# Kernel tuning notes

Hardware: AMD Instinct MI355X
Metric: run time of the kernel (lower is better)

Reference implementation:

```python
import jax, jax.numpy as jnp
import numpy as np

B, H, W = 4, 128, 128
DIM, HEADS, WS, SS = 192, 6, 16, 8
CAT, NTOK, RD, DTD = 128, 64, 10, 64
MLPH, KSZ = 384, 5
LN_EPS = 1e-5


def _ln(x, g, b):
    mu = jnp.mean(x, axis=-1, keepdims=True)
    var = jnp.mean((x - mu) ** 2, axis=-1, keepdims=True)
    return (x - mu) * jax.lax.rsqrt(var + LN_EPS) * g + b


def _l2n(x):
    n = jnp.sqrt(jnp.sum(x * x, axis=-1, keepdims=True))
    return x / jnp.maximum(n, 1e-12)


def _win_part(x, ws):
    b, h, w, c = x.shape
    x = x.reshape(b, h // ws, ws, w // ws, ws, c).transpose(0, 1, 3, 2, 4, 5)
    return x.reshape(-1, ws, ws, c)


def _win_rev(win, ws, h, w):
    b = win.shape[0] // ((h // ws) * (w // ws))
    x = win.reshape(b, h // ws, w // ws, ws, ws, -1).transpose(0, 1, 3, 2, 4, 5)
    return x.reshape(b, h, w, -1)


def _make_rpi(ws):
    coords = np.stack(np.meshgrid(np.arange(ws), np.arange(ws), indexing='ij'))
    cf = coords.reshape(2, -1)
    rel = (cf[:, :, None] - cf[:, None, :]).transpose(1, 2, 0)
    rel[:, :, 0] += ws - 1
    rel[:, :, 1] += ws - 1
    rel[:, :, 0] *= 2 * ws - 1
    return rel.sum(-1)


def _make_attn_mask(h, w, ws, ss):
    img = np.zeros((1, h, w, 1), np.float32)
    cnt = 0
    for hs in (slice(0, -ws), slice(-ws, -ss), slice(-ss, None)):
        for vs in (slice(0, -ws), slice(-ws, -ss), slice(-ss, None)):
            img[:, hs, vs, :] = cnt
            cnt += 1
    mw = img.reshape(1, h // ws, ws, w // ws, ws, 1).transpose(0, 1, 3, 2, 4, 5).reshape(-1, ws * ws)
    am = mw[:, None, :] - mw[:, :, None]
    return np.where(am != 0, -100.0, 0.0).astype(np.float32)


def _fwd(x, td, attn_mask, rpi, h, w, norm1_g, norm1_b, norm2_g, norm2_b,
         wqkv_w, wqkv_b, wq_w, wq_b, wk_w, wk_b, wv_w, wv_b, atd_scale,
         aca_proj_w, aca_proj_b, rpb_table, win_proj_w, win_proj_b,
         fc_td_w, fc_td_b, fc1_w, fc1_b, dw_w, dw_b, fc2_w, fc2_b):
    b, n, c = x.shape
    shortcut = x
    xn = _ln(x, norm1_g, norm1_b)
    qkv = xn @ wqkv_w + wqkv_b  # (b, n, 3c)

    # --- ATD_CA: normalized cross-attention to token dictionary ---
    q = xn @ wq_w + wq_b          # (b, n, RD)
    k = td @ wk_w + wk_b          # (b, m, RD)
    v = td @ wv_w + wv_b          # (b, m, c)
    sim = jnp.einsum('bnr,bmr->bnm', _l2n(q), _l2n(k))
    scale = 1.0 + jnp.clip(atd_scale, 0.0, 3.0) * np.log(NTOK)
    sim = jax.nn.softmax(sim * scale, axis=-1)
    x_atd = sim @ v               # (b, n, c)

    # --- AC_MSA: category-sorted grouped attention ---
    tk_id = jnp.argmax(sim, axis=-1)                 # (b, n) int
    gs = min(n, CAT)
    ng = (n + gs - 1) // gs
    pad_n = ng * gs - n
    sidx = jnp.argsort(tk_id, axis=-1)
    inv = jnp.argsort(sidx, axis=-1)                 # inverse permutation
    sqkv = jnp.take_along_axis(qkv, sidx[:, :, None], axis=1)
    if pad_n > 0:
        sqkv = jnp.concatenate([sqkv, jnp.flip(sqkv[:, n - pad_n:n, :], axis=1)], axis=1)
    hd = c // HEADS
    g = sqkv.reshape(b, ng, gs, 3, HEADS, hd).transpose(3, 0, 1, 4, 2, 5)
    qg, kg, vg = g[0], g[1], g[2]
    ga = jax.nn.softmax(jnp.einsum('bghqd,bghkd->bghqk', qg, kg) * (hd ** -0.5), axis=-1)
    yg = jnp.einsum('bghqk,bghkd->bghqd', ga, vg).transpose(0, 1, 3, 2, 4).reshape(b, ng * gs, c)[:, :n]
    x_aca = jnp.take_along_axis(yg, inv[:, :, None], axis=1) @ aca_proj_w + aca_proj_b

    # --- per-token gathered token-dict features for the FFN ---
    td_f = td @ fc_td_w + fc_td_b                    # (b, m, DTD)
    x_td = jnp.take_along_axis(td_f, jnp.broadcast_to(tk_id[:, :, None], (b, n, DTD)), axis=1)

    # --- shifted window attention over qkv ---
    qkv_img = qkv.reshape(b, h, w, 3 * c)
    sh = jnp.roll(qkv_img, shift=(-SS, -SS), axis=(1, 2))
    xw = _win_part(sh, WS).reshape(-1, WS * WS, 3 * c)
    b_, nn_ = xw.shape[0], WS * WS
    wq3 = xw.reshape(b_, nn_, 3, HEADS, hd).transpose(2, 0, 3, 1, 4)
    qw, kw, vw = wq3[0] * (hd ** -0.5), wq3[1], wq3[2]
    aw = jnp.einsum('bhqd,bhkd->bhqk', qw, kw)
    rpb = rpb_table[rpi.reshape(-1)].reshape(nn_, nn_, HEADS).transpose(2, 0, 1)
    aw = aw + rpb[None]
    nw = attn_mask.shape[0]
    aw = (aw.reshape(b_ // nw, nw, HEADS, nn_, nn_) + attn_mask[None, :, None]).reshape(b_, HEADS, nn_, nn_)
    aw = jax.nn.softmax(aw, axis=-1)
    yw = jnp.einsum('bhqk,bhkd->bhqd', aw, vw).transpose(0, 2, 1, 3).reshape(b_, nn_, c)
    yw = yw @ win_proj_w + win_proj_b
    yw = _win_rev(yw.reshape(-1, WS, WS, c), WS, h, w)
    x_win = jnp.roll(yw, shift=(SS, SS), axis=(1, 2)).reshape(b, n, c)

    x = shortcut + x_win + x_atd + x_aca

    # --- ConvFFN with concatenated token-dict features + depthwise conv ---
    xn2 = _ln(x, norm2_g, norm2_b)
    x1 = jax.nn.gelu(xn2 @ fc1_w + fc1_b, approximate=False)
    xc = jnp.concatenate([x1, x_td], axis=-1)        # (b, n, MLPH+DTD)
    ch = MLPH + DTD
    img = xc.reshape(b, h, w, ch)
    cv = jax.lax.conv_general_dilated(img, dw_w, (1, 1), 'SAME',
                                      dimension_numbers=('NHWC', 'HWIO', 'NHWC'),
                                      feature_group_count=ch)
    cv = jax.nn.gelu(cv + dw_b, approximate=False).reshape(b, n, ch)
    x = x + (xc + cv) @ fc2_w + fc2_b
    return x


def setup_inputs():
    key = jax.random.key(0)
    ks = jax.random.split(key, 16)
    w02 = lambda k, s: jax.random.normal(k, s, jnp.float32) * 0.02
    return {
        'x': jax.random.normal(ks[0], (B, H * W, DIM), jnp.float32),
        'td': jax.random.normal(ks[1], (B, NTOK, DIM), jnp.float32),
        'attn_mask': jnp.asarray(_make_attn_mask(H, W, WS, SS)),
        'rpi': jnp.asarray(_make_rpi(WS), jnp.int32),
        'h': H, 'w': W,
        'norm1_g': jnp.ones((DIM,)), 'norm1_b': jnp.zeros((DIM,)),
        'norm2_g': jnp.ones((DIM,)), 'norm2_b': jnp.zeros((DIM,)),
        'wqkv_w': w02(ks[2], (DIM, 3 * DIM)), 'wqkv_b': jnp.zeros((3 * DIM,)),
        'wq_w': w02(ks[3], (DIM, RD)), 'wq_b': jnp.zeros((RD,)),
        'wk_w': w02(ks[4], (DIM, RD)), 'wk_b': jnp.zeros((RD,)),
        'wv_w': w02(ks[5], (DIM, DIM)), 'wv_b': jnp.zeros((DIM,)),
        'atd_scale': jnp.ones((1,)),
        'aca_proj_w': w02(ks[6], (DIM, DIM)), 'aca_proj_b': jnp.zeros((DIM,)),
        'rpb_table': w02(ks[7], ((2 * WS - 1) ** 2, HEADS)),
        'win_proj_w': w02(ks[8], (DIM, DIM)), 'win_proj_b': jnp.zeros((DIM,)),
        'fc_td_w': w02(ks[9], (DIM, DTD)), 'fc_td_b': jnp.zeros((DTD,)),
        'fc1_w': w02(ks[10], (DIM, MLPH)), 'fc1_b': jnp.zeros((MLPH,)),
        'dw_w': w02(ks[11], (KSZ, KSZ, 1, MLPH + DTD)), 'dw_b': jnp.zeros((MLPH + DTD,)),
        'fc2_w': w02(ks[12], (MLPH + DTD, DIM)), 'fc2_b': jnp.zeros((DIM,)),
    }


def reference(x, td, attn_mask, rpi, h, w, norm1_g, norm1_b, norm2_g, norm2_b,
              wqkv_w, wqkv_b, wq_w, wq_b, wk_w, wk_b, wv_w, wv_b, atd_scale,
              aca_proj_w, aca_proj_b, rpb_table, win_proj_w, win_proj_b,
              fc_td_w, fc_td_b, fc1_w, fc1_b, dw_w, dw_b, fc2_w, fc2_b):
    return _fwd(x, td, attn_mask, rpi, h, w, norm1_g, norm1_b, norm2_g, norm2_b,
                wqkv_w, wqkv_b, wq_w, wq_b, wk_w, wk_b, wv_w, wv_b, atd_scale,
                aca_proj_w, aca_proj_b, rpb_table, win_proj_w, win_proj_b,
                fc_td_w, fc_td_b, fc1_w, fc1_b, dw_w, dw_b, fc2_w, fc2_b)
```

## Files before the change

### kernel.cpp

```cpp
#include <hip/hip_runtime.h>
#include <hip/hip_bf16.h>
#include <math.h>

typedef __hip_bfloat16 bf16;
typedef short bf16x8 __attribute__((ext_vector_type(8)));
typedef float f32x4 __attribute__((ext_vector_type(4)));

#define NB 4
#define HH 128
#define WWID 128
#define CC 192
#define NPB (HH*WWID)
#define NT (NB*NPB)
#define NHEADS 6
#define HD 32
#define NTOK 64
#define RDIM 10
#define DTD 64
#define MLPH 384
#define CHF (MLPH+DTD)

__device__ __forceinline__ float b2f(bf16 v){ return __bfloat162float(v); }
__device__ __forceinline__ bf16  f2b(float v){ return __float2bfloat16(v); }
__device__ __forceinline__ float bfu(unsigned short u){ return __uint_as_float(((unsigned)u)<<16); }
__device__ __forceinline__ float geluf(float v){ return 0.5f*v*(1.0f+erff(v*0.70710678118654752f)); }
__device__ __forceinline__ int rg3(int v){ return v<112?0:(v<120?1:2); }

__device__ __forceinline__ float wsumf(float v){
  #pragma unroll
  for (int m=32;m>0;m>>=1) v += __shfl_xor(v,m);
  return v;
}

__global__ void k_sentinel(float* out, int n, float v){
  int i = blockIdx.x*256+threadIdx.x;
  if (i<n) out[i]=v;
}

template<int BF16IN>
__global__ __launch_bounds__(256) void k_ln(const float* __restrict__ xf, const bf16* __restrict__ xb,
                                            const float* __restrict__ g, const float* __restrict__ be,
                                            bf16* __restrict__ out){
  int wave = threadIdx.x>>6, lane = threadIdx.x&63;
  int tok = blockIdx.x*4 + wave;
  size_t base = (size_t)tok*CC;
  float v0,v1,v2;
  if (BF16IN){ v0=b2f(xb[base+lane]); v1=b2f(xb[base+lane+64]); v2=b2f(xb[base+lane+128]); }
  else { v0=xf[base+lane]; v1=xf[base+lane+64]; v2=xf[base+lane+128]; }
  float s = wsumf(v0+v1+v2);
  float mu = s*(1.0f/192.0f);
  float d0=v0-mu, d1=v1-mu, d2=v2-mu;
  float q = wsumf(d0*d0+d1*d1+d2*d2);
  float rs = rsqrtf(q*(1.0f/192.0f)+1e-5f);
  out[base+lane]     = f2b(d0*rs*g[lane]     + be[lane]);
  out[base+lane+64]  = f2b(d1*rs*g[lane+64]  + be[lane+64]);
  out[base+lane+128] = f2b(d2*rs*g[lane+128] + be[lane+128]);
}

__global__ __launch_bounds__(256) void k_wt(const float* __restrict__ W, bf16* __restrict__ Wt, int K, int N){
  int i = blockIdx.x*256+threadIdx.x;
  if (i < K*N){ int n = i / K, k = i - n*K; Wt[i] = f2b(W[(size_t)k*N + n]); }
}

__global__ __launch_bounds__(64) void k_kn(const float* __restrict__ td, const float* __restrict__ wk,
                                           const float* __restrict__ wkb, double* __restrict__ kn){
  int t = blockIdx.x*64+threadIdx.x;
  double kk[10]; double sq=0.0;
  const float* tr = td + (size_t)t*CC;
  #pragma unroll
  for (int r=0;r<10;r++) kk[r]=(double)wkb[r];
  for (int k=0;k<CC;k++){
    double tv=(double)tr[k];
    #pragma unroll
    for (int r=0;r<10;r++) kk[r] += tv*(double)wk[k*10+r];
  }
  #pragma unroll
  for (int r=0;r<10;r++) sq += kk[r]*kk[r];
  double inv = 1.0/fmax(sqrt(sq),1e-12);
  #pragma unroll
  for (int r=0;r<10;r++) kn[t*10+r]=kk[r]*inv;
}

__global__ __launch_bounds__(256) void k_v(const float* __restrict__ td, const float* __restrict__ wv,
                                           const float* __restrict__ wvb, float* __restrict__ vb){
  int idx = blockIdx.x*256+threadIdx.x;
  int c = idx % CC; int bm = idx / CC;
  const float* tr = td + (size_t)bm*CC;
  float a = wvb[c];
  for (int k=0;k<CC;k++) a = fmaf(tr[k], wv[(size_t)k*CC+c], a);
  vb[idx] = a;
}

__global__ __launch_bounds__(256) void k_tdf(const float* __restrict__ td, const float* __restrict__ w,
                                             const float* __restrict__ bb, float* __restrict__ tdf){
  int idx = blockIdx.x*256+threadIdx.x;
  int d = idx & 63; int bm = idx >> 6;
  const float* tr = td + (size_t)bm*CC;
  float a = bb[d];
  for (int k=0;k<CC;k++) a = fmaf(tr[k], w[(size_t)k*64+d], a);
  tdf[idx] = a;
}

__global__ __launch_bounds__(256) void k_rpbq(const int* __restrict__ rpi, const float* __restrict__ rpbt,
                                              bf16* __restrict__ rpbq){
  int idx = blockIdx.x*256+threadIdx.x;
  int h = idx>>16; int qk = idx&65535;
  rpbq[idx] = f2b(rpbt[rpi[qk]*6 + h]);
}

__global__ __launch_bounds__(256) void k_sim(const float* __restrict__ x, const float* __restrict__ n1g,
                                             const float* __restrict__ n1b, const float* __restrict__ wq,
                                             const float* __restrict__ wqb, const double* __restrict__ kn,
                                             const float* __restrict__ atds,
                                             float* __restrict__ sim, int* __restrict__ tkid){
  int wave = threadIdx.x>>6, lane = threadIdx.x&63;
  int tok = blockIdx.x*4 + wave;
  const float* xr = x + (size_t)tok*CC;
  double v0=(double)xr[lane], v1=(double)xr[lane+64], v2=(double)xr[lane+128];
  double s = v0+v1+v2;
  double s2 = v0*v0+v1*v1+v2*v2;
  #pragma unroll
  for (int m=32;m>0;m>>=1){ s += __shfl_xor(s,m); s2 += __shfl_xor(s2,m); }
  double mu = s*(1.0/192.0);
  double var = s2*(1.0/192.0) - mu*mu;
  double rs = 1.0/sqrt(var+1e-5);
  double xn0 = (v0-mu)*rs*(double)n1g[lane]     + (double)n1b[lane];
  double xn1 = (v1-mu)*rs*(double)n1g[lane+64]  + (double)n1b[lane+64];
  double xn2 = (v2-mu)*rs*(double)n1g[lane+128] + (double)n1b[lane+128];
  double q[10]; double sq=0.0;
  #pragma unroll
  for (int r=0;r<10;r++){
    double a = xn0*(double)wq[lane*10+r] + xn1*(double)wq[(lane+64)*10+r] + xn2*(double)wq[(lane+128)*10+r];
    #pragma unroll
    for (int m=32;m>0;m>>=1) a += __shfl_xor(a,m);
    a += (double)wqb[r];
    q[r]=a; sq += a*a;
  }
  double inv = 1.0/fmax(sqrt(sq),1e-12);
  int b = tok>>14;
  const double* kr = kn + ((size_t)((b<<6)+lane))*10;
  double dot=0.0;
  #pragma unroll
  for (int r=0;r<10;r++) dot += q[r]*kr[r];
  dot *= inv;
  double bv=dot; int bi=lane;
  #pragma unroll
  for (int m=32;m>0;m>>=1){
    double ov=__shfl_xor(bv,m); int oi=__shfl_xor(bi,m);
    if (ov>bv || (ov==bv && oi<bi)){ bv=ov; bi=oi; }
  }
  if (lane==0) tkid[tok]=bi;
  double asd = fmin(fmax((double)atds[0],0.0),3.0);
  float t = (float)(dot*(1.0 + asd*4.1588830833596715));
  float mx=t;
  #pragma unroll
  for (int m=32;m>0;m>>=1) mx = fmaxf(mx,__shfl_xor(mx,m));
  float pp = __expf(t-mx);
  float ssf = pp;
  #pragma unroll
  for (int m=32;m>0;m>>=1) ssf += __shfl_xor(ssf,m);
  sim[(size_t)tok*64+lane] = pp/ssf;
}

template<int K, int KC, int NS, int ACT, int OUTMODE>
__global__ __launch_bounds__(256) void k_mm(const bf16* __restrict__ A, const bf16* __restrict__ Wt,
                                            const float* __restrict__ bias, const void* __restrict__ aux,
                                            void* __restrict__ outp){
  __shared__ __align__(16) char As[64*KC*2];
  __shared__ __align__(16) char Ws[64*KC*2];
  int row0 = blockIdx.x*64, n0 = blockIdx.y*64;
  int ti = threadIdx.x;
  int wave = ti>>6, lane = ti&63, g = lane>>4, l15 = lane&15;
  f32x4 acc[4];
  #pragma unroll
  for (int mt=0;mt<4;mt++){ f32x4 z={0.f,0.f,0.f,0.f}; acc[mt]=z; }
  const int KC8 = KC/8;
  for (int c0=0; c0<K; c0+=KC){
    if (c0) __syncthreads();
    for (int u=ti; u<64*KC8; u+=256){
      int r = u/KC8, kc = u-r*KC8;
      uint4 va = *(const uint4*)(A  + (size_t)(row0+r)*K + c0 + kc*8);
      *(uint4*)(As + ((r*(KC*2) + kc*16) ^ ((r&7)<<4))) = va;
      uint4 vw = *(const uint4*)(Wt + (size_t)(n0+r)*K + c0 + kc*8);
      *(uint4*)(Ws + ((r*(KC*2) + kc*16) ^ ((r&7)<<4))) = vw;
    }
    __syncthreads();
    #pragma unroll
    for (int ks=0; ks<KC/32; ks++){
      int rw = wave*16 + l15;
      bf16x8 bfr = *(const bf16x8*)(Ws + ((rw*(KC*2) + ks*64 + g*16) ^ ((rw&7)<<4)));
      #pragma unroll
      for (int mt=0;mt<4;mt++){
        int ra = mt*16 + l15;
        bf16x8 af = *(const bf16x8*)(As + ((ra*(KC*2) + ks*64 + g*16) ^ ((ra&7)<<4)));
        acc[mt] = __builtin_amdgcn_mfma_f32_16x16x32_bf16(af, bfr, acc[mt], 0,0,0);
      }
    }
  }
  int col = n0 + wave*16 + l15;
  float bb = bias[col];
  #pragma unroll
  for (int mt=0;mt<4;mt++){
    #pragma unroll
    for (int j=0;j<4;j++){
      int row = row0 + mt*16 + g*4 + j;
      float v = acc[mt][j] + bb;
      if (OUTMODE==0){
        ((bf16*)outp)[(size_t)row*NS + col] = f2b(ACT ? geluf(v) : v);
      } else if (OUTMODE==2){
        size_t o = (size_t)row*NS + col;
        ((float*)outp)[o] = b2f(((const bf16*)aux)[o]) + v;
      } else if (OUTMODE==3){
        int win=row>>8, tii=row&255;
        int b=win>>6, wloc=win&63;
        int wy=wloc>>3, wx=wloc&7, tyy=tii>>4, txx=tii&15;
        int oy=(wy*16+tyy+8)&127, ox=(wx*16+txx+8)&127;
        size_t o=((size_t)(b*NPB + oy*128 + ox))*NS + col;
        ((bf16*)outp)[o] = f2b(((const float*)aux)[o] + v);
      } else {
        int orow=(row & ~(NPB-1)) + ((const int*)aux)[row];
        size_t o=(size_t)orow*NS + col;
        bf16* xo=(bf16*)outp;
        xo[o] = f2b(b2f(xo[o]) + v);
      }
    }
  }
}

__device__ __forceinline__ float ldw(const bf16* p, size_t i){ return __bfloat162float(p[i]); }
__device__ __forceinline__ float ldw(const float* p, size_t i){ return p[i]; }

template<int KD, int CB, typename WT>
__device__ __forceinline__ void gemm_core(const float (*As)[KD], const WT* __restrict__ W, int N, float (&acc)[8][CB]){
  int tid = threadIdx.x;
  for (int k=0;k<KD;k+=4){
    float w0[CB],w1[CB],w2[CB],w3[CB];
    #pragma unroll
    for (int j=0;j<CB;j++){
      int c = tid + 64*j;
      w0[j]=ldw(W,(size_t)(k+0)*N+c);
      w1[j]=ldw(W,(size_t)(k+1)*N+c);
      w2[j]=ldw(W,(size_t)(k+2)*N+c);
      w3[j]=ldw(W,(size_t)(k+3)*N+c);
    }
    #pragma unroll
    for (int r=0;r<8;r++){
      float4 a = *reinterpret_cast<const float4*>(&As[r][k]);
      #pragma unroll
      for (int j=0;j<CB;j++)
        acc[r][j]=fmaf(a.x,w0[j],fmaf(a.y,w1[j],fmaf(a.z,w2[j],fmaf(a.w,w3[j],acc[r][j]))));
    }
  }
}

__global__ __launch_bounds__(64) void k_xatd(const float* __restrict__ sim, const float* __restrict__ vb,
                                             bf16* __restrict__ xacc){
  __shared__ __align__(16) float As[8][64];
  int row0=blockIdx.x*8;
  for (int idx=threadIdx.x; idx<8*64; idx+=64){
    int r=idx>>6, k=idx&63;
    As[r][k]=sim[(size_t)(row0+r)*64+k];
  }
  __syncthreads();
  float acc[8][3]={};
  const float* Wv = vb + (size_t)(row0>>14)*64*CC;
  gemm_core<64,3>(As, Wv, CC, acc);
  int tid=threadIdx.x;
  #pragma unroll
  for (int j=0;j<3;j++){
    int c=tid+64*j;
    #pragma unroll
    for (int r=0;r<8;r++){
      size_t o=(size_t)(row0+r)*CC+c;
      xacc[o]=f2b(b2f(xacc[o])+acc[r][j]);
    }
  }
}

__global__ __launch_bounds__(256) void k_tdgather(const float* __restrict__ tdf, const int* __restrict__ tkid,
                                                  bf16* __restrict__ xc){
  int idx = blockIdx.x*256+threadIdx.x;
  int d = idx & 63; int tok = idx >> 6;
  int b = tok >> 14;
  int m = tkid[tok];
  xc[(size_t)tok*CHF + MLPH + d] = f2b(tdf[((size_t)((b<<6)+m))*64 + d]);
}

__global__ __launch_bounds__(256) void k_hist(const int* __restrict__ tkid, int* __restrict__ chist){
  __shared__ int h[64];
  int b = blockIdx.x>>6, ch = blockIdx.x&63;
  if (threadIdx.x<64) h[threadIdx.x]=0;
  __syncthreads();
  int v = tkid[b*NPB + ch*256 + threadIdx.x];
  atomicAdd(&h[v],1);
  __syncthreads();
  if (threadIdx.x<64) chist[(size_t)blockIdx.x*64 + threadIdx.x] = h[threadIdx.x];
}

__global__ __launch_bounds__(64) void k_scan(const int* __restrict__ chist, int* __restrict__ coff,
                                             int* __restrict__ bstart){
  int b = blockIdx.x; int v = threadIdx.x;
  __shared__ int tot[64], bs[64];
  int s=0;
  for (int ch=0; ch<64; ch++){
    coff[((size_t)(b*64+ch))*64+v] = s;
    s += chist[((size_t)(b*64+ch))*64+v];
  }
  tot[v]=s;
  __syncthreads();
  if (v==0){ int run=0; for (int u=0;u<64;u++){ bs[u]=run; run+=tot[u]; } }
  __syncthreads();
  bstart[b*64+v] = bs[v];
}

__global__ __launch_bounds__(256) void k_place(const int* __restrict__ tkid, const int* __restrict__ coff,
                                               const int* __restrict__ bstart, int* __restrict__ sidx){
  __shared__ int vals[256];
  int b = blockIdx.x>>6, ch = blockIdx.x&63;
  int tid = threadIdx.x;
  int tok = ch*256 + tid;
  int v = tkid[b*NPB + tok];
  vals[tid]=v;
  __syncthreads();
  int lr=0;
  for (int j=0;j<tid;j++) lr += (vals[j]==v);
  int pos = bstart[b*64+v] + coff[((size_t)(b*64+ch))*64+v] + lr;
  sidx[b*NPB + pos] = tok;
}

__global__ __launch_bounds__(256,4) void k_acattn(const bf16* __restrict__ qkv, const int* __restrict__ sidx,
                                                  bf16* __restrict__ yg){
  __shared__ bf16 Kl[128*32];
  __shared__ bf16 Vt[32*128];
  __shared__ bf16 Ps[4][16*32];
  int bid=blockIdx.x;
  int h = bid % NHEADS; int gg = (bid/NHEADS) & 127; int b = bid/(NHEADS*128);
  int ti = threadIdx.x;
  if (ti < 128){
    int srow = b*NPB + sidx[b*NPB + gg*128 + ti];
    const bf16* src = qkv + (size_t)srow*576 + 192 + h*32;
    const uint4* s4 = (const uint4*)src;
    char* kb = (char*)Kl;
    #pragma unroll
    for (int w=0;w<4;w++) *(uint4*)(kb + ((ti*64 + w*16) ^ ((ti&7)<<4))) = s4[w];
    const bf16* vsrc = src + 192;
    char* vbp = (char*)Vt;
    #pragma unroll
    for (int d=0;d<32;d++) *(bf16*)(vbp + ((d*256 + ti*2) ^ ((d&7)<<4))) = vsrc[d];
  }
  __syncthreads();
  int wave=ti>>6, lane=ti&63, g=lane>>4, l15=lane&15;
  bf16x8 qf[2];
  #pragma unroll
  for (int qt=0;qt<2;qt++){
    int q = wave*32 + qt*16 + l15;
    int srow = b*NPB + sidx[b*NPB + gg*128 + q];
    qf[qt] = *(const bf16x8*)(qkv + (size_t)srow*576 + h*32 + g*8);
  }
  f32x4 O[2][2]; float lsp[2][4];
  #pragma unroll
  for (int qt=0;qt<2;qt++){
    #pragma unroll
    for (int dt=0;dt<2;dt++){ f32x4 z={0.f,0.f,0.f,0.f}; O[qt][dt]=z; }
    #pragma unroll
    for (int j=0;j<4;j++) lsp[qt][j]=0.f;
  }
  const float rsc=0.17677669529663687f;
  const char* kb=(const char*)Kl; const char* vbp=(const char*)Vt;
  for (int st=0; st<4; st++){
    int r0=st*32+l15, r1=st*32+16+l15;
    bf16x8 kf0 = *(const bf16x8*)(kb + ((r0*64 + g*16) ^ ((r0&7)<<4)));
    bf16x8 kf1 = *(const bf16x8*)(kb + ((r1*64 + g*16) ^ ((r1&7)<<4)));
    int d0=l15, d1=16+l15;
    bf16x8 vf0 = *(const bf16x8*)(vbp + ((d0*256 + st*64 + g*16) ^ ((d0&7)<<4)));
    bf16x8 vf1 = *(const bf16x8*)(vbp + ((d1*256 + st*64 + g*16) ^ ((d1&7)<<4)));
    #pragma unroll
    for (int qt=0;qt<2;qt++){
      f32x4 z={0.f,0.f,0.f,0.f};
      f32x4 s0 = __builtin_amdgcn_mfma_f32_16x16x32_bf16(qf[qt], kf0, z, 0,0,0);
      f32x4 s1 = __builtin_amdgcn_mfma_f32_16x16x32_bf16(qf[qt], kf1, z, 0,0,0);
      float p0[4],p1[4];
      char* pb=(char*)Ps[wave];
      #pragma unroll
      for (int j=0;j<4;j++){
        p0[j]=__expf(fminf(s0[j]*rsc,80.f));
        p1[j]=__expf(fminf(s1[j]*rsc,80.f));
        lsp[qt][j]+=p0[j]+p1[j];
        int q=g*4+j;
        *(bf16*)(pb + ((q*64 + l15*2) ^ ((q&7)<<4)))      = f2b(p0[j]);
        *(bf16*)(pb + ((q*64 + 32 + l15*2) ^ ((q&7)<<4))) = f2b(p1[j]);
      }
      bf16x8 pa = *(const bf16x8*)((const char*)Ps[wave] + ((l15*64 + g*16) ^ ((l15&7)<<4)));
      O[qt][0]=__builtin_amdgcn_mfma_f32_16x16x32_bf16(pa, vf0, O[qt][0], 0,0,0);
      O[qt][1]=__builtin_amdgcn_mfma_f32_16x16x32_bf16(pa, vf1, O[qt][1], 0,0,0);
    }
  }
  #pragma unroll
  for (int qt=0;qt<2;qt++){
    #pragma unroll
    for (int msk=1; msk<16; msk<<=1){
      #pragma unroll
      for (int j=0;j<4;j++) lsp[qt][j]+=__shfl_xor(lsp[qt][j],msk);
    }
    #pragma unroll
    for (int j=0;j<4;j++){
      float inv=1.0f/lsp[qt][j];
      int q = wave*32 + qt*16 + g*4 + j;
      bf16* yo = yg + ((size_t)(b*NPB + gg*128 + q))*CC + h*32;
      yo[l15]    = f2b(O[qt][0][j]*inv);
      yo[16+l15] = f2b(O[qt][1][j]*inv);
    }
  }
}

__global__ __launch_bounds__(256,3) void k_winattn(const bf16* __restrict__ qkv, const bf16* __restrict__ rpbq,
                                                   bf16* __restrict__ yw){
  __shared__ bf16 Kl[256*32];
  __shared__ bf16 Vt[32*256];
  __shared__ bf16 Ps[4][16*32];
  int bid = blockIdx.x;
  int h = bid % NHEADS; int win = bid / NHEADS;
  int b = win >> 6; int wloc = win & 63;
  int wy = wloc >> 3, wx = wloc & 7;
  int ti = threadIdx.x;
  {
    int ty=ti>>4, tx=ti&15;
    int oy=(wy*16+ty+8)&127, ox=(wx*16+tx+8)&127;
    const bf16* src = qkv + (size_t)(b*NPB+oy*128+ox)*576 + 192 + h*32;
    const uint4* s4 = (const uint4*)src;
    char* kb = (char*)Kl;
    #pragma unroll
    for (int w=0;w<4;w++) *(uint4*)(kb + ((ti*64 + w*16) ^ ((ti&7)<<4))) = s4[w];
    const bf16* vsrc = src + 192;
    char* vbp = (char*)Vt;
    #pragma unroll
    for (int d=0;d<32;d++) *(bf16*)(vbp + ((d*512 + ti*2) ^ ((d&7)<<4))) = vsrc[d];
  }
  __syncthreads();
  int wave=ti>>6, lane=ti&63, g=lane>>4, l15=lane&15;
  bf16x8 qf[4];
  #pragma unroll
  for (int qt=0;qt<4;qt++){
    int ty=wave*4+qt, tx=l15;
    int oy=(wy*16+ty+8)&127, ox=(wx*16+tx+8)&127;
    qf[qt] = *(const bf16x8*)(qkv + (size_t)(b*NPB+oy*128+ox)*576 + h*32 + g*8);
  }
  f32x4 O[4][2]; float lsp[4][4];
  #pragma unroll
  for (int qt=0;qt<4;qt++){
    #pragma unroll
    for (int dt=0;dt<2;dt++){ f32x4 z={0.f,0.f,0.f,0.f}; O[qt][dt]=z; }
    #pragma unroll
    for (int j=0;j<4;j++) lsp[qt][j]=0.f;
  }
  const float rsc=0.17677669529663687f;
  int rxk = rg3(wx*16+l15);
  int rxq[4], ryq[4];
  #pragma unroll
  for (int j=0;j<4;j++) rxq[j]=rg3(wx*16+g*4+j);
  #pragma unroll
  for (int qt=0;qt<4;qt++) ryq[qt]=rg3(wy*16+wave*4+qt);
  const char* kb=(const char*)Kl; const char* vbp=(const char*)Vt;
  for (int st=0; st<8; st++){
    int r0=st*32+l15, r1=st*32+16+l15;
    bf16x8 kf0 = *(const bf16x8*)(kb + ((r0*64 + g*16) ^ ((r0&7)<<4)));
    bf16x8 kf1 = *(const bf16x8*)(kb + ((r1*64 + g*16) ^ ((r1&7)<<4)));
    int d0=l15, d1=16+l15;
    bf16x8 vf0 = *(const bf16x8*)(vbp + ((d0*512 + st*64 + g*16) ^ ((d0&7)<<4)));
    bf16x8 vf1 = *(const bf16x8*)(vbp + ((d1*512 + st*64 + g*16) ^ ((d1&7)<<4)));
    int rk0 = rg3(wy*16+st*2)*3   + rxk;
    int rk1 = rg3(wy*16+st*2+1)*3 + rxk;
    #pragma unroll
    for (int qt=0;qt<4;qt++){
      f32x4 z={0.f,0.f,0.f,0.f};
      f32x4 s0 = __builtin_amdgcn_mfma_f32_16x16x32_bf16(qf[qt], kf0, z, 0,0,0);
      f32x4 s1 = __builtin_amdgcn_mfma_f32_16x16x32_bf16(qf[qt], kf1, z, 0,0,0);
      int qr0 = wave*64 + qt*16 + g*4;
      float p0[4],p1[4];
      char* pb=(char*)Ps[wave];
      #pragma unroll
      for (int j=0;j<4;j++){
        const bf16* rb = rpbq + (((size_t)h*256 + qr0 + j)<<8) + st*32;
        int rq = ryq[qt]*3 + rxq[j];
        float b0 = b2f(rb[l15])    + (rq!=rk0 ? -100.f : 0.f);
        float b1 = b2f(rb[16+l15]) + (rq!=rk1 ? -100.f : 0.f);
        p0[j]=__expf(fminf(fmaf(s0[j],rsc,b0),80.f));
        p1[j]=__expf(fminf(fmaf(s1[j],rsc,b1),80.f));
        lsp[qt][j]+=p0[j]+p1[j];
        int q=g*4+j;
        *(bf16*)(pb + ((q*64 + l15*2) ^ ((q&7)<<4)))      = f2b(p0[j]);
        *(bf16*)(pb + ((q*64 + 32 + l15*2) ^ ((q&7)<<4))) = f2b(p1[j]);
      }
      bf16x8 pa = *(const bf16x8*)((const char*)Ps[wave] + ((l15*64 + g*16) ^ ((l15&7)<<4)));
      O[qt][0]=__builtin_amdgcn_mfma_f32_16x16x32_bf16(pa, vf0, O[qt][0], 0,0,0);
      O[qt][1]=__builtin_amdgcn_mfma_f32_16x16x32_bf16(pa, vf1, O[qt][1], 0,0,0);
    }
  }
  #pragma unroll
  for (int qt=0;qt<4;qt++){
    #pragma unroll
    for (int msk=1; msk<16; msk<<=1){
      #pragma unroll
      for (int j=0;j<4;j++) lsp[qt][j]+=__shfl_xor(lsp[qt][j],msk);
    }
    #pragma unroll
    for (int j=0;j<4;j++){
      float inv=1.0f/lsp[qt][j];
      int q = wave*64 + qt*16 + g*4 + j;
      bf16* yo = yw + ((size_t)win*256 + q)*CC + h*32;
      yo[l15]    = f2b(O[qt][0][j]*inv);
      yo[16+l15] = f2b(O[qt][1][j]*inv);
    }
  }
}

__global__ __launch_bounds__(256,4) void k_dw(const bf16* __restrict__ xc, const float* __restrict__ dww,
                                              const float* __restrict__ dwb, bf16* __restrict__ sv){
  int tid = blockIdx.x*256 + threadIdx.x;
  int ch8 = tid % 56; int pt = tid / 56;
  int x0 = (pt & 31)*4; int yq = (pt>>5)&127; int b = pt>>12;
  float acc[4][8];
  #pragma unroll
  for (int p=0;p<4;p++)
    #pragma unroll
    for (int c=0;c<8;c++) acc[p][c]=0.f;
  unsigned choff = (unsigned)ch8*8;
  const float* wp = dww + choff;
  #pragma unroll
  for (int dy=0;dy<5;dy++){
    int yy = yq+dy-2;
    if ((unsigned)yy>127u) continue;
    float4 w0[5], w1[5];
    #pragma unroll
    for (int dx=0;dx<5;dx++){
      w0[dx] = *(const float4*)(wp + (dy*5+dx)*CHF);
      w1[dx] = *(const float4*)(wp + (dy*5+dx)*CHF + 4);
    }
    unsigned rowoff = ((unsigned)(b<<14) + ((unsigned)yy<<7))*CHF + choff;
    #pragma unroll
    for (int j=0;j<8;j++){
      int ox = x0-2+j;
      if ((unsigned)ox>127u) continue;
      uint4 v = *(const uint4*)(xc + rowoff + (unsigned)ox*CHF);
      float u[8];
      unsigned vv[4]={v.x,v.y,v.z,v.w};
      #pragma unroll
      for (int t=0;t<4;t++){
        u[2*t]  = __uint_as_float(vv[t]<<16);
        u[2*t+1]= __uint_as_float(vv[t]&0xffff0000u);
      }
      #pragma unroll
      for (int dx=0;dx<5;dx++){
        int p = j-dx;
        if (p<0 || p>3) continue;
        acc[p][0]=fmaf(u[0],w0[dx].x,acc[p][0]);
        acc[p][1]=fmaf(u[1],w0[dx].y,acc[p][1]);
        acc[p][2]=fmaf(u[2],w0[dx].z,acc[p][2]);
        acc[p][3]=fmaf(u[3],w0[dx].w,acc[p][3]);
        acc[p][4]=fmaf(u[4],w1[dx].x,acc[p][4]);
        acc[p][5]=fmaf(u[5],w1[dx].y,acc[p][5]);
        acc[p][6]=fmaf(u[6],w1[dx].z,acc[p][6]);
        acc[p][7]=fmaf(u[7],w1[dx].w,acc[p][7]);
      }
    }
  }
  float4 b0 = *(const float4*)(dwb + choff);
  float4 b1 = *(const float4*)(dwb + choff + 4);
  float bb[8]={b0.x,b0.y,b0.z,b0.w,b1.x,b1.y,b1.z,b1.w};
  unsigned obase = ((unsigned)(b<<14) + ((unsigned)yq<<7) + (unsigned)x0)*CHF + choff;
  #pragma unroll
  for (int p=0;p<4;p++){
    uint4 cv4 = *(const uint4*)(xc + obase + (unsigned)p*CHF);
    unsigned vv[4]={cv4.x,cv4.y,cv4.z,cv4.w};
    bf16 o[8];
    #pragma unroll
    for (int t=0;t<4;t++){
      float c0 = __uint_as_float(vv[t]<<16);
      float c1 = __uint_as_float(vv[t]&0xffff0000u);
      o[2*t]   = f2b(c0 + geluf(acc[p][2*t]  + bb[2*t]));
      o[2*t+1] = f2b(c1 + geluf(acc[p][2*t+1]+ bb[2*t+1]));
    }
    *(uint4*)(sv + obase + (unsigned)p*CHF) = *(const uint4*)o;
  }
}

extern "C" void kernel_launch(void* const* d_in, const int* in_sizes, int n_in,
                              void* d_out, int out_size, void* d_ws, size_t ws_size,
                              hipStream_t stream){
  const float* x    = (const float*)d_in[0];
  const float* td   = (const float*)d_in[1];
  const int*   rpi  = (const int*)d_in[3];
  const float* n1g  = (const float*)d_in[6];
  const float* n1b  = (const float*)d_in[7];
  const float* n2g  = (const float*)d_in[8];
  const float* n2b  = (const float*)d_in[9];
  const float* wqkv = (const float*)d_in[10];
  const float* wqkvb= (const float*)d_in[11];
  const float* wq   = (const float*)d_in[12];
  const float* wqb  = (const float*)d_in[13];
  const float* wk   = (const float*)d_in[14];
  const float* wkb  = (const float*)d_in[15];
  const float* wv   = (const float*)d_in[16];
  const float* wvb  = (const float*)d_in[17];
  const float* atds = (const float*)d_in[18];
  const float* acaw = (const float*)d_in[19];
  const float* acab = (const float*)d_in[20];
  const float* rpbt = (const float*)d_in[21];
  const float* winw = (const float*)d_in[22];
  const float* winb = (const float*)d_in[23];
  const float* tdw  = (const float*)d_in[24];
  const float* tdbb = (const float*)d_in[25];
  const float* f1w  = (const float*)d_in[26];
  const float* f1b  = (const float*)d_in[27];
  const float* dww  = (const float*)d_in[28];
  const float* dwb  = (const float*)d_in[29];
  const float* f2w  = (const float*)d_in[30];
  const float* f2bb = (const float*)d_in[31];
  float* out = (float*)d_out;

  const size_t QKV_BYTES = (size_t)NT*576*2;
  const size_t XN_BYTES  = (size_t)NT*CC*2;
  const size_t XC_BYTES  = (size_t)NT*CHF*2;

  char* base = (char*)d_ws;
  size_t off = 0;
  auto give = [&](size_t bytes)->char*{
    off = (off + 255) & ~(size_t)255;
    char* r = base + off; off += bytes; return r;
  };
  char*   qkv_r = give(QKV_BYTES);
  char*   xn_r  = give(XN_BYTES);
  char*   sim_r = give(XN_BYTES);
  bf16*   xacc  = (bf16*)  give(XN_BYTES);
  int*    tkid  = (int*)   give((size_t)NT*4);
  int*    sidx  = (int*)   give((size_t)NT*4);
  double* kn    = (double*)give((size_t)NB*64*RDIM*8);
  float*  vbuf  = (float*) give((size_t)NB*64*CC*4);
  float*  tdf   = (float*) give((size_t)NB*64*DTD*4);
  int*    chist = (int*)   give((size_t)NB*64*64*4);
  int*    coff  = (int*)   give((size_t)NB*64*64*4);
  int*    bstart= (int*)   give((size_t)NB*64*4);
  bf16*   rpbq  = (bf16*)  give((size_t)NHEADS*256*256*2);
  bf16*   wqkvt = (bf16*)  give((size_t)192*576*2);
  bf16*   f1wt  = (bf16*)  give((size_t)192*384*2);
  bf16*   f2wt  = (bf16*)  give((size_t)448*192*2);
  bf16*   winwt = (bf16*)  give((size_t)192*192*2);
  bf16*   acawt = (bf16*)  give((size_t)192*192*2);

  if (off > ws_size){
    k_sentinel<<<(out_size+255)/256,256,0,stream>>>(out, out_size, (float)(ws_size>>20));
    return;
  }

  bf16*  qkv  = (bf16*)qkv_r;
  bf16*  xc   = (bf16*)qkv_r;
  bf16*  sv   = (bf16*)(qkv_r + XC_BYTES);
  bf16*  xn   = (bf16*)xn_r;
  bf16*  atmp = (bf16*)xn_r;
  float* sim  = (float*)sim_r;

  k_wt<<<(192*576+255)/256,256,0,stream>>>(wqkv, wqkvt, 192, 576);
  k_wt<<<(192*384+255)/256,256,0,stream>>>(f1w, f1wt, 192, 384);
  k_wt<<<(448*192+255)/256,256,0,stream>>>(f2w, f2wt, 448, 192);
  k_wt<<<(192*192+255)/256,256,0,stream>>>(winw, winwt, 192, 192);
  k_wt<<<(192*192+255)/256,256,0,stream>>>(acaw, acawt, 192, 192);
  k_ln<0><<<NT/4,256,0,stream>>>(x, nullptr, n1g, n1b, xn);
  k_mm<192,192,576,0,0><<<dim3(NT/64,9),256,0,stream>>>(xn, wqkvt, wqkvb, nullptr, qkv);
  k_rpbq<<<NHEADS*256*256/256,256,0,stream>>>(rpi, rpbt, rpbq);
  k_winattn<<<NB*64*NHEADS,256,0,stream>>>(qkv, rpbq, atmp);
  k_mm<192,192,192,0,3><<<dim3(NT/64,3),256,0,stream>>>(atmp, winwt, winb, x, xacc);
  k_kn<<<4,64,0,stream>>>(td, wk, wkb, kn);
  k_v<<<(NB*64*CC)/256,256,0,stream>>>(td, wv, wvb, vbuf);
  k_tdf<<<(NB*64*DTD)/256,256,0,stream>>>(td, tdw, tdbb, tdf);
  k_sim<<<NT/4,256,0,stream>>>(x, n1g, n1b, wq, wqb, kn, atds, sim, tkid);
  k_hist<<<NB*64,256,0,stream>>>(tkid, chist);
  k_scan<<<NB,64,0,stream>>>(chist, coff, bstart);
  k_place<<<NB*64,256,0,stream>>>(tkid, coff, bstart, sidx);
  k_acattn<<<NB*128*NHEADS,256,0,stream>>>(qkv, sidx, atmp);
  k_mm<192,192,192,0,4><<<dim3(NT/64,3),256,0,stream>>>(atmp, acawt, acab, sidx, xacc);
  k_xatd<<<NT/8,64,0,stream>>>(sim, vbuf, xacc);
  k_tdgather<<<NT*64/256,256,0,stream>>>(tdf, tkid, xc);
  k_ln<1><<<NT/4,256,0,stream>>>(nullptr, xacc, n2g, n2b, xn);
  k_mm<192,192,448,1,0><<<dim3(NT/64,6),256,0,stream>>>(xn, f1wt, f1b, nullptr, xc);
  k_dw<<<NT*56/4/256,256,0,stream>>>(xc, dww, dwb, sv);
  k_mm<448,224,192,0,2><<<dim3(NT/64,3),256,0,stream>>>(sv, f2wt, f2bb, xacc, out);
}
```

Baseline: 611.6 us.

## Restructure sim kernel: fold LayerNorm into query weights, tile 64 tokens per block

Precomputes gamma-scaled query weights and bias sums so the normalized query projection becomes rs*(x·gw - mu*S1) + S2, with no per-element normalization. The sim kernel now stages 64 tokens in shared memory and assigns one wave per rank dimension, which removes the per-rank full-wave shuffle reductions. The softmax max-subtraction is dropped because the logits are bounded cosine similarities times a clamped scale. The cost is a large shared-memory footprint and a 640-thread block, which may lower occupancy, plus small fp64 rounding differences.

```diff
diff --git a/kernel.cpp b/kernel.cpp
--- a/kernel.cpp
+++ b/kernel.cpp
@@ -62,6 +62,25 @@
   if (i < K*N){ int n = i / K, k = i - n*K; Wt[i] = f2b(W[(size_t)k*N + n]); }
 }
 
+__global__ __launch_bounds__(256) void k_gw(const float* __restrict__ n1g, const float* __restrict__ n1b,
+                                            const float* __restrict__ wq, const float* __restrict__ wqb,
+                                            double* __restrict__ gw, double* __restrict__ S12){
+  int ti=threadIdx.x;
+  for (int i=ti;i<1920;i+=256){
+    int c=i/10;
+    gw[i]=(double)n1g[c]*(double)wq[i];
+  }
+  if (ti<10){
+    double s1=0.0,s2=0.0;
+    for (int c=0;c<192;c++){
+      double w=(double)wq[c*10+ti];
+      s1=fma((double)n1g[c],w,s1);
+      s2=fma((double)n1b[c],w,s2);
+    }
+    S12[ti]=s1; S12[10+ti]=s2+(double)wqb[ti];
+  }
+}
+
 __global__ __launch_bounds__(64) void k_kn(const float* __restrict__ td, const float* __restrict__ wk,
                                            const float* __restrict__ wkb, double* __restrict__ kn){
   int t = blockIdx.x*64+threadIdx.x;
@@ -108,58 +127,77 @@
   rpbq[idx] = f2b(rpbt[rpi[qk]*6 + h]);
 }
 
-__global__ __launch_bounds__(256) void k_sim(const float* __restrict__ x, const float* __restrict__ n1g,
-                                             const float* __restrict__ n1b, const float* __restrict__ wq,
-                                             const float* __restrict__ wqb, const double* __restrict__ kn,
+__global__ __launch_bounds__(640) void k_sim(const float* __restrict__ x, const double* __restrict__ gw,
+                                             const double* __restrict__ S12, const double* __restrict__ kn,
                                              const float* __restrict__ atds,
                                              float* __restrict__ sim, int* __restrict__ tkid){
-  int wave = threadIdx.x>>6, lane = threadIdx.x&63;
-  int tok = blockIdx.x*4 + wave;
-  const float* xr = x + (size_t)tok*CC;
-  double v0=(double)xr[lane], v1=(double)xr[lane+64], v2=(double)xr[lane+128];
-  double s = v0+v1+v2;
-  double s2 = v0*v0+v1*v1+v2*v2;
-  #pragma unroll
-  for (int m=32;m>0;m>>=1){ s += __shfl_xor(s,m); s2 += __shfl_xor(s2,m); }
-  double mu = s*(1.0/192.0);
-  double var = s2*(1.0/192.0) - mu*mu;
-  double rs = 1.0/sqrt(var+1e-5);
-  double xn0 = (v0-mu)*rs*(double)n1g[lane]     + (double)n1b[lane];
-  double xn1 = (v1-mu)*rs*(double)n1g[lane+64]  + (double)n1b[lane+64];
-  double xn2 = (v2-mu)*rs*(double)n1g[lane+128] + (double)n1b[lane+128];
-  double q[10]; double sq=0.0;
-  #pragma unroll
-  for (int r=0;r<10;r++){
-    double a = xn0*(double)wq[lane*10+r] + xn1*(double)wq[(lane+64)*10+r] + xn2*(double)wq[(lane+128)*10+r];
-    #pragma unroll
-    for (int m=32;m>0;m>>=1) a += __shfl_xor(a,m);
-    a += (double)wqb[r];
-    q[r]=a; sq += a*a;
-  }
-  double inv = 1.0/fmax(sqrt(sq),1e-12);
-  int b = tok>>14;
-  const double* kr = kn + ((size_t)((b<<6)+lane))*10;
-  double dot=0.0;
-  #pragma unroll
-  for (int r=0;r<10;r++) dot += q[r]*kr[r];
-  dot *= inv;
-  double bv=dot; int bi=lane;
-  #pragma unroll
-  for (int m=32;m>0;m>>=1){
-    double ov=__shfl_xor(bv,m); int oi=__shfl_xor(bi,m);
-    if (ov>bv || (ov==bv && oi<bi)){ bv=ov; bi=oi; }
-  }
-  if (lane==0) tkid[tok]=bi;
-  double asd = fmin(fmax((double)atds[0],0.0),3.0);
-  float t = (float)(dot*(1.0 + asd*4.1588830833596715));
-  float mx=t;
-  #pragma unroll
-  for (int m=32;m>0;m>>=1) mx = fmaxf(mx,__shfl_xor(mx,m));
-  float pp = __expf(t-mx);
-  float ssf = pp;
-  #pragma unroll
-  for (int m=32;m>0;m>>=1) ssf += __shfl_xor(ssf,m);
-  sim[(size_t)tok*64+lane] = pp/ssf;
+  __shared__ float xs[64][193];
+  __shared__ double muv[64], rsv[64];
+  __shared__ double ql[64][10];
+  int ti = threadIdx.x;
+  int blk = blockIdx.x;
+  size_t gbase = (size_t)blk*64*192;
+  for (int i=ti; i<64*192; i+=640){
+    int tok=i/192, c=i-tok*192;
+    xs[tok][c] = x[gbase+i];
+  }
+  __syncthreads();
+  int wave = ti>>6, lane = ti&63;
+  if (wave==0){
+    double s0=0,s1=0,t0=0,t1=0;
+    #pragma unroll 4
+    for (int c=0;c<192;c+=2){
+      double v0=(double)xs[lane][c], v1=(double)xs[lane][c+1];
+      s0+=v0; s1+=v1; t0=fma(v0,v0,t0); t1=fma(v1,v1,t1);
+    }
+    double s=s0+s1, s2=t0+t1;
+    double mu=s*(1.0/192.0);
+    double var=s2*(1.0/192.0)-mu*mu;
+    muv[lane]=mu; rsv[lane]=1.0/sqrt(var+1e-5);
+  }
+  __syncthreads();
+  {
+    int r = wave;
+    double mu=muv[lane], rs=rsv[lane];
+    double a0=0,a1=0;
+    #pragma unroll 4
+    for (int c=0;c<192;c+=2){
+      a0 = fma((double)xs[lane][c],   gw[c*10+r],     a0);
+      a1 = fma((double)xs[lane][c+1], gw[(c+1)*10+r], a1);
+    }
+    ql[lane][r] = rs*((a0+a1) - mu*S12[r]) + S12[10+r];
+  }
+  __syncthreads();
+  int b = blk>>8;
+  double kr[10];
+  #pragma unroll
+  for (int r2=0;r2<10;r2++) kr[r2]=kn[((size_t)(b*64+lane))*10+r2];
+  double asd=fmin(fmax((double)atds[0],0.0),3.0);
+  double scl=1.0+asd*4.1588830833596715;
+  for (int tk=wave; tk<64; tk+=10){
+    double dot=0.0, sq=0.0;
+    #pragma unroll
+    for (int r2=0;r2<10;r2++){
+      double qv=ql[tk][r2];
+      dot=fma(qv,kr[r2],dot);
+      sq =fma(qv,qv,sq);
+    }
+    dot *= 1.0/fmax(sqrt(sq),1e-12);
+    double bv=dot; int bi=lane;
+    #pragma unroll
+    for (int m2=32;m2>0;m2>>=1){
+      double ov=__shfl_xor(bv,m2); int oi=__shfl_xor(bi,m2);
+      if (ov>bv || (ov==bv && oi<bi)){ bv=ov; bi=oi; }
+    }
+    int tokg = blk*64+tk;
+    if (lane==0) tkid[tokg]=bi;
+    float t=(float)(dot*scl);
+    float pp=__expf(t);
+    float ssf=pp;
+    #pragma unroll
+    for (int m2=32;m2>0;m2>>=1) ssf+=__shfl_xor(ssf,m2);
+    sim[(size_t)tokg*64+lane]=pp/ssf;
+  }
 }
 
 template<int K, int KC, int NS, int ACT, int OUTMODE>
@@ -646,6 +684,8 @@
   bf16*   f2wt  = (bf16*)  give((size_t)448*192*2);
   bf16*   winwt = (bf16*)  give((size_t)192*192*2);
   bf16*   acawt = (bf16*)  give((size_t)192*192*2);
+  double* gw    = (double*)give((size_t)1920*8);
+  double* S12   = (double*)give((size_t)20*8);
 
   if (off > ws_size){
     k_sentinel<<<(out_size+255)/256,256,0,stream>>>(out, out_size, (float)(ws_size>>20));
@@ -664,6 +704,7 @@
   k_wt<<<(448*192+255)/256,256,0,stream>>>(f2w, f2wt, 448, 192);
   k_wt<<<(192*192+255)/256,256,0,stream>>>(winw, winwt, 192, 192);
   k_wt<<<(192*192+255)/256,256,0,stream>>>(acaw, acawt, 192, 192);
+  k_gw<<<1,256,0,stream>>>(n1g, n1b, wq, wqb, gw, S12);
   k_ln<0><<<NT/4,256,0,stream>>>(x, nullptr, n1g, n1b, xn);
   k_mm<192,192,576,0,0><<<dim3(NT/64,9),256,0,stream>>>(xn, wqkvt, wqkvb, nullptr, qkv);
   k_rpbq<<<NHEADS*256*256/256,256,0,stream>>>(rpi, rpbt, rpbq);
@@ -672,7 +713,7 @@
   k_kn<<<4,64,0,stream>>>(td, wk, wkb, kn);
   k_v<<<(NB*64*CC)/256,256,0,stream>>>(td, wv, wvb, vbuf);
   k_tdf<<<(NB*64*DTD)/256,256,0,stream>>>(td, tdw, tdbb, tdf);
-  k_sim<<<NT/4,256,0,stream>>>(x, n1g, n1b, wq, wqb, kn, atds, sim, tkid);
+  k_sim<<<NT/64,640,0,stream>>>(x, gw, S12, kn, atds, sim, tkid);
   k_hist<<<NB*64,256,0,stream>>>(tkid, chist);
   k_scan<<<NB,64,0,stream>>>(chist, coff, bstart);
   k_place<<<NB*64,256,0,stream>>>(tkid, coff, bstart, sidx);
```

New measurement: 597.7 us. 1.02x faster.
